# Kernel optimization log

Measured on AMD Instinct MI355X. Metric: run time of the kernel, lower is better.

Reference implementation:

```python
import jax, jax.numpy as jnp
import numpy as np

N = 100000       # nodes
E = 3200000      # edges
D_IN, D_CONV, D_LIN, D_OUT = 32, 16, 64, 4


def _uniform(k, shape, fan_in):
    s = 1.0 / np.sqrt(fan_in)
    return jax.random.uniform(k, shape, jnp.float32, -s, s)


def setup_inputs() -> dict:
    key = jax.random.key(0)
    ks = jax.random.split(key, 32)
    inp = {}
    inp["x"] = jax.random.normal(ks[0], (N, D_IN), jnp.float32)
    inp["edge_index"] = jax.random.randint(ks[1], (2, E), 0, N).astype(jnp.int64)
    conv_dims = [(D_IN, D_CONV), (D_CONV, D_CONV), (D_CONV, D_CONV)]
    j = 2
    for i, (di, do) in enumerate(conv_dims):
        inp[f"Wl{i}"] = _uniform(ks[j], (di, do), di); j += 1  # neighbor lin (lin_l)
        inp[f"Wr{i}"] = _uniform(ks[j], (di, do), di); j += 1  # root lin (lin_r, no bias)
        inp[f"bl{i}"] = _uniform(ks[j], (do,), di); j += 1
    lin_dims = [(D_CONV, D_LIN), (D_LIN, D_LIN), (D_LIN, D_LIN), (D_LIN, D_OUT)]
    for i, (di, do) in enumerate(lin_dims):
        inp[f"LW{i}"] = _uniform(ks[j], (di, do), di); j += 1
        inp[f"LB{i}"] = _uniform(ks[j], (do,), di); j += 1
    return inp


def _sage_conv(x, src, dst, Wl, Wr, b):
    # mean aggregation of source-node features at destination nodes
    msg_sum = jax.ops.segment_sum(x[src], dst, num_segments=N)          # [N, d_in]
    deg = jax.ops.segment_sum(jnp.ones((src.shape[0], 1), x.dtype), dst, num_segments=N)
    agg = msg_sum / jnp.maximum(deg, 1.0)
    return agg @ Wl + b + x @ Wr


def reference(x, edge_index,
              Wl0, Wr0, bl0, Wl1, Wr1, bl1, Wl2, Wr2, bl2,
              LW0, LB0, LW1, LB1, LW2, LB2, LW3, LB3):
    src, dst = edge_index[0], edge_index[1]
    # conv stack (dropout is identity in eval mode)
    for Wl, Wr, b in ((Wl0, Wr0, bl0), (Wl1, Wr1, bl1), (Wl2, Wr2, bl2)):
        x = jax.nn.elu(_sage_conv(x, src, dst, Wl, Wr, b))
    # hidden linear stack
    for W, b in ((LW0, LB0), (LW1, LB1), (LW2, LB2)):
        x = jax.nn.elu(x @ W + b)
    return x @ LW3 + LB3
```

## Files before the change

### kernel.cpp

```cpp
#include <hip/hip_runtime.h>
#include <hip/hip_fp16.h>
#include <math.h>

#define DCONV 16
#define BSH 8
#define GPART 512
#define GSH 9
#define MAXNB 512
#define SCAP 6912
#define FCAP 12288


__global__ void __launch_bounds__(512) k_hist(const int* __restrict__ ei, int E,
                                              int nb_buckets, int chunk,
                                              int* __restrict__ cnt) {
  __shared__ int hist[MAXNB];
  int g = blockIdx.x;
  for (int i = threadIdx.x; i < nb_buckets; i += 512) hist[i] = 0;
  __syncthreads();
  int e0 = g * chunk, e1 = min(e0 + chunk, E);
  for (int e = e0 + threadIdx.x; e < e1; e += 512)
    atomicAdd(&hist[ei[E + e] >> BSH], 1);
  __syncthreads();
  for (int i = threadIdx.x; i < nb_buckets; i += 512)
    cnt[i * GPART + g] = hist[i];
}

__global__ void k_block_sums(const int* __restrict__ in, int n, int* __restrict__ part) {
  int i = blockIdx.x * 256 + threadIdx.x;
  int v = (i < n) ? in[i] : 0;
  #pragma unroll
  for (int off = 32; off > 0; off >>= 1) v += __shfl_down(v, off, 64);
  __shared__ int ws[4];
  if ((threadIdx.x & 63) == 0) ws[threadIdx.x >> 6] = v;
  __syncthreads();
  if (threadIdx.x == 0) part[blockIdx.x] = ws[0] + ws[1] + ws[2] + ws[3];
}

__global__ void k_scan_part(int* __restrict__ part, int nb) {
  __shared__ int s[1024];
  int t = threadIdx.x;
  int v = (t < nb) ? part[t] : 0;
  s[t] = v;
  __syncthreads();
  for (int off = 1; off < 1024; off <<= 1) {
    int u = (t >= off) ? s[t - off] : 0;
    __syncthreads();
    s[t] += u;
    __syncthreads();
  }
  if (t < nb) part[t] = s[t] - v;
}

__global__ void k_excl_apply(const int* __restrict__ in, int n, const int* __restrict__ part,
                             int* __restrict__ outT, int nb_buckets) {
  __shared__ int s[256];
  int t = threadIdx.x;
  int i = blockIdx.x * 256 + t;
  int v = (i < n) ? in[i] : 0;
  s[t] = v;
  __syncthreads();
  for (int off = 1; off < 256; off <<= 1) {
    int u = (t >= off) ? s[t - off] : 0;
    __syncthreads();
    s[t] += u;
    __syncthreads();
  }
  if (i < n) {
    int excl = s[t] - v + part[blockIdx.x];
    int b = i >> GSH;
    int g = i & (GPART - 1);
    outT[g * nb_buckets + b] = excl;
  }
}

__global__ void __launch_bounds__(512) k_scatter(const int* __restrict__ ei, int E,
                                                 int nb_buckets, int chunk,
                                                 const int* __restrict__ offT,
                                                 int* __restrict__ temp) {
  __shared__ int sh[512];
  __shared__ int lofs[MAXNB];
  __shared__ int lcur[MAXNB];
  __shared__ int gbase[MAXNB];
  __shared__ int sorted[SCAP];
  __shared__ unsigned short sbkt[SCAP];
  int g = blockIdx.x, t = threadIdx.x;
  int e0 = g * chunk, e1 = min(e0 + chunk, E);
  int total = e1 - e0;

  if (total > SCAP) {
    for (int i = t; i < nb_buckets; i += 512) lcur[i] = offT[(size_t)g * nb_buckets + i];
    __syncthreads();
    for (int e = e0 + t; e < e1; e += 512) {
      int s = ei[e];
      int d = ei[E + e];
      int b = d >> BSH;
      int pos = atomicAdd(&lcur[b], 1);
      temp[pos] = (s << BSH) | (d & ((1 << BSH) - 1));
    }
    return;
  }

  lcur[t] = 0;
  __syncthreads();
  for (int e = e0 + t; e < e1; e += 512)
    atomicAdd(&lcur[ei[E + e] >> BSH], 1);
  __syncthreads();
  int v = (t < nb_buckets) ? lcur[t] : 0;
  sh[t] = v;
  __syncthreads();
  for (int off = 1; off < 512; off <<= 1) {
    int u = (t >= off) ? sh[t - off] : 0;
    __syncthreads();
    sh[t] += u;
    __syncthreads();
  }
  if (t < nb_buckets) {
    int excl = sh[t] - v;
    lofs[t] = excl;
    lcur[t] = excl;
    gbase[t] = offT[(size_t)g * nb_buckets + t];
  }
  __syncthreads();
  for (int e = e0 + t; e < e1; e += 512) {
    int s = ei[e];
    int d = ei[E + e];
    int b = d >> BSH;
    int pos = atomicAdd(&lcur[b], 1);
    sorted[pos] = (s << BSH) | (d & ((1 << BSH) - 1));
    sbkt[pos] = (unsigned short)b;
  }
  __syncthreads();
  for (int i = t; i < total; i += 512) {
    int b = sbkt[i];
    temp[gbase[b] + (i - lofs[b])] = sorted[i];
  }
}

__global__ void __launch_bounds__(512) k_fine(const int* __restrict__ temp,
                                              const int* __restrict__ offT,
                                              int nb_buckets, int E, int n,
                                              int* __restrict__ rowptr, int* __restrict__ csr) {
  __shared__ int hist[1 << BSH];
  __shared__ int cur[1 << BSH];
  __shared__ int sorted[FCAP];
  int b = blockIdx.x, t = threadIdx.x;
  int lo = offT[b];
  int hi = (b == nb_buckets - 1) ? E : offT[b + 1];
  int cntb = hi - lo;
  if (t < 256) hist[t] = 0;
  __syncthreads();
  for (int e = lo + t; e < hi; e += 512)
    atomicAdd(&hist[temp[e] & 255], 1);
  __syncthreads();
  int v = 0;
  if (t < 256) { v = hist[t]; cur[t] = v; }
  __syncthreads();
  for (int offm = 1; offm < 256; offm <<= 1) {
    int u = (t >= offm && t < 256) ? cur[t - offm] : 0;
    __syncthreads();
    if (t < 256) cur[t] += u;
    __syncthreads();
  }
  bool inlds = (cntb <= FCAP);
  if (t < 256) {
    int excl = cur[t] - v;
    int node = (b << BSH) + t;
    if (node < n) rowptr[node] = lo + excl;
    cur[t] = inlds ? excl : (lo + excl);
  }
  if (b == nb_buckets - 1 && t == 0) rowptr[n] = hi;
  __syncthreads();
  if (inlds) {
    for (int e = lo + t; e < hi; e += 512) {
      int p = temp[e];
      int pos = atomicAdd(&cur[p & 255], 1);
      sorted[pos] = p >> BSH;
    }
    __syncthreads();
    for (int i = t; i < cntb; i += 512) csr[lo + i] = sorted[i];
  } else {
    for (int e = lo + t; e < hi; e += 512) {
      int p = temp[e];
      int pos = atomicAdd(&cur[p & 255], 1);
      csr[pos] = p >> BSH;
    }
  }
}


__global__ void k_xform32h(const float* __restrict__ xin,
                           const float* __restrict__ Wl,
                           __half* __restrict__ y, int n) {
  __shared__ float sWl[32 * 16];
  int t = threadIdx.x;
  for (int i = t; i < 32 * 16; i += 256) sWl[i] = Wl[i];
  __syncthreads();
  int l = t & 15;
  int base = (t & 63) & ~15;
  int node = (blockIdx.x * 256 + t) >> 4;
  if (node >= n) return;
  float x0 = xin[node * 32 + l];
  float x1 = xin[node * 32 + 16 + l];
  float ay = 0.f;
  #pragma unroll
  for (int i = 0; i < 16; ++i) {
    float v0 = __shfl(x0, base + i, 64);
    float v1 = __shfl(x1, base + i, 64);
    ay += v0 * sWl[i * 16 + l] + v1 * sWl[(16 + i) * 16 + l];
  }
  y[node * 16 + l] = __float2half_rn(ay);
}

__global__ void k_xform16h(const float* __restrict__ hin,
                           const float* __restrict__ Wl,
                           __half* __restrict__ y, int n) {
  __shared__ float sWl[16 * 16];
  int t = threadIdx.x;
  for (int i = t; i < 16 * 16; i += 256) sWl[i] = Wl[i];
  __syncthreads();
  int l = t & 15;
  int base = (t & 63) & ~15;
  int node = (blockIdx.x * 256 + t) >> 4;
  if (node >= n) return;
  float x0 = hin[node * 16 + l];
  float ay = 0.f;
  #pragma unroll
  for (int i = 0; i < 16; ++i) {
    float v0 = __shfl(x0, base + i, 64);
    ay += v0 * sWl[i * 16 + l];
  }
  y[node * 16 + l] = __float2half_rn(ay);
}


template <int DI>
__global__ void k_agg(const __half* __restrict__ y, const float* __restrict__ hin,
                      const float* __restrict__ Wr, const float* __restrict__ bias,
                      const int* __restrict__ rowptr, const int* __restrict__ csr,
                      float* __restrict__ outp, int n) {
  __shared__ __align__(16) float sWr[DI * 16];
  __shared__ float sb[16];
  {
    int tt = threadIdx.x;
    for (int i = tt; i < DI * 16; i += 256) sWr[i] = Wr[i];
    if (tt < 16) sb[tt] = bias[tt];
  }
  __syncthreads();

  int t = blockIdx.x * 256 + threadIdx.x;
  int l = t & 3;
  int h = (t >> 2) & 1;
  int node = t >> 3;
  if (node >= n) return;
  int r0 = rowptr[node], r1 = rowptr[node + 1];
  int deg = r1 - r0;
  int halfn = (deg + 1) >> 1;
  int ks = r0 + h * halfn;
  int ke = h ? r1 : (r0 + halfn);

  const uint2* __restrict__ yv = reinterpret_cast<const uint2*>(y);

  float a0 = 0.f, a1 = 0.f, a2 = 0.f, a3 = 0.f;
  float b0 = 0.f, b1 = 0.f, b2 = 0.f, b3 = 0.f;
  float c0 = 0.f, c1 = 0.f, c2 = 0.f, c3 = 0.f;
  float d0 = 0.f, d1 = 0.f, d2 = 0.f, d3 = 0.f;
  int k = ks;
  for (; k + 3 < ke; k += 4) {
    int ia = csr[k], ib = csr[k + 1], ic = csr[k + 2], id = csr[k + 3];
    uint2 ra = yv[ia * 4 + l];
    uint2 rb = yv[ib * 4 + l];
    uint2 rc = yv[ic * 4 + l];
    uint2 rd = yv[id * 4 + l];
    float2 fa0 = __half22float2(*reinterpret_cast<const __half2*>(&ra.x));
    float2 fa1 = __half22float2(*reinterpret_cast<const __half2*>(&ra.y));
    float2 fb0 = __half22float2(*reinterpret_cast<const __half2*>(&rb.x));
    float2 fb1 = __half22float2(*reinterpret_cast<const __half2*>(&rb.y));
    float2 fc0 = __half22float2(*reinterpret_cast<const __half2*>(&rc.x));
    float2 fc1 = __half22float2(*reinterpret_cast<const __half2*>(&rc.y));
    float2 fd0 = __half22float2(*reinterpret_cast<const __half2*>(&rd.x));
    float2 fd1 = __half22float2(*reinterpret_cast<const __half2*>(&rd.y));
    a0 += fa0.x; a1 += fa0.y; a2 += fa1.x; a3 += fa1.y;
    b0 += fb0.x; b1 += fb0.y; b2 += fb1.x; b3 += fb1.y;
    c0 += fc0.x; c1 += fc0.y; c2 += fc1.x; c3 += fc1.y;
    d0 += fd0.x; d1 += fd0.y; d2 += fd1.x; d3 += fd1.y;
  }
  for (; k < ke; ++k) {
    int ia = csr[k];
    uint2 ra = yv[ia * 4 + l];
    float2 fa0 = __half22float2(*reinterpret_cast<const __half2*>(&ra.x));
    float2 fa1 = __half22float2(*reinterpret_cast<const __half2*>(&ra.y));
    a0 += fa0.x; a1 += fa0.y; a2 += fa1.x; a3 += fa1.y;
  }
  float s0 = a0 + b0 + c0 + d0;
  float s1 = a1 + b1 + c1 + d1;
  float s2 = a2 + b2 + c2 + d2;
  float s3 = a3 + b3 + c3 + d3;

  int cbase = l * 4;
  float4 rr;
  if (h == 0) rr = *reinterpret_cast<const float4*>(&sb[cbase]);
  else        rr = make_float4(0.f, 0.f, 0.f, 0.f);
  const int HD = DI / 2;
  #pragma unroll
  for (int i = 0; i < HD; ++i) {
    int ii = h * HD + i;
    float hv = hin[node * DI + ii];
    float4 w = *reinterpret_cast<const float4*>(&sWr[ii * 16 + cbase]);
    rr.x += hv * w.x; rr.y += hv * w.y; rr.z += hv * w.z; rr.w += hv * w.w;
  }

  s0 += __shfl_xor(s0, 4, 64);
  s1 += __shfl_xor(s1, 4, 64);
  s2 += __shfl_xor(s2, 4, 64);
  s3 += __shfl_xor(s3, 4, 64);
  rr.x += __shfl_xor(rr.x, 4, 64);
  rr.y += __shfl_xor(rr.y, 4, 64);
  rr.z += __shfl_xor(rr.z, 4, 64);
  rr.w += __shfl_xor(rr.w, 4, 64);

  if (h == 0) {
    float inv = 1.f / fmaxf((float)deg, 1.f);
    float ax = s0 * inv + rr.x;
    float ay = s1 * inv + rr.y;
    float az = s2 * inv + rr.z;
    float aw = s3 * inv + rr.w;
    float4 o;
    o.x = ax > 0.f ? ax : (__expf(ax) - 1.f);
    o.y = ay > 0.f ? ay : (__expf(ay) - 1.f);
    o.z = az > 0.f ? az : (__expf(az) - 1.f);
    o.w = aw > 0.f ? aw : (__expf(aw) - 1.f);
    *reinterpret_cast<float4*>(&outp[node * 16 + cbase]) = o;
  }
}


typedef _Float16 f16x4 __attribute__((ext_vector_type(4)));
typedef float f32x4 __attribute__((ext_vector_type(4)));

#define MFMA16(a, b, c) __builtin_amdgcn_mfma_f32_16x16x16f16(a, b, c, 0, 0, 0)
#define CSTRIDE 20

__global__ void __launch_bounds__(256) k_mlp(
    const float* __restrict__ xin,
    const float* __restrict__ W0, const float* __restrict__ B0,
    const float* __restrict__ W1, const float* __restrict__ B1,
    const float* __restrict__ W2, const float* __restrict__ B2,
    const float* __restrict__ W3, const float* __restrict__ B3,
    float* __restrict__ out, int n, int nchunks) {
  __shared__ __align__(16) _Float16 hbuf[4][2][64 * CSTRIDE];
  int t = threadIdx.x;
  int w = t >> 6;
  int lane = t & 63;
  int row = lane & 15;
  int kg = lane >> 4;

  f16x4 b0f[4], b1f[4][4], b2f[4][4], b3f[4];
  float bs0[4], bs1v[4], bs2v[4];
  #pragma unroll
  for (int nt = 0; nt < 4; ++nt) {
    #pragma unroll
    for (int j = 0; j < 4; ++j)
      b0f[nt][j] = (_Float16)W0[(kg * 4 + j) * 64 + nt * 16 + row];
    bs0[nt] = B0[nt * 16 + row];
    bs1v[nt] = B1[nt * 16 + row];
    bs2v[nt] = B2[nt * 16 + row];
  }
  #pragma unroll
  for (int ks = 0; ks < 4; ++ks)
    #pragma unroll
    for (int nt = 0; nt < 4; ++nt)
      #pragma unroll
      for (int j = 0; j < 4; ++j) {
        b1f[ks][nt][j] = (_Float16)W1[(ks * 16 + kg * 4 + j) * 64 + nt * 16 + row];
        b2f[ks][nt][j] = (_Float16)W2[(ks * 16 + kg * 4 + j) * 64 + nt * 16 + row];
      }
  #pragma unroll
  for (int ks = 0; ks < 4; ++ks)
    #pragma unroll
    for (int j = 0; j < 4; ++j)
      b3f[ks][j] = (row < 4) ? (_Float16)W3[(ks * 16 + kg * 4 + j) * 4 + row]
                             : (_Float16)0.f;
  float bs3 = (row < 4) ? B3[row] : 0.f;

  _Float16* hb0 = &hbuf[w][0][0];
  _Float16* hb1 = &hbuf[w][1][0];

  for (int c = blockIdx.x; c < nchunks; c += gridDim.x) {
    int nodeBase = c * 64 + w * 16;
    if (nodeBase >= n) continue;

    int nd = nodeBase + row;
    if (nd >= n) nd = n - 1;
    float4 xv = *reinterpret_cast<const float4*>(&xin[nd * 16 + kg * 4]);
    f16x4 a0;
    a0[0] = (_Float16)xv.x; a0[1] = (_Float16)xv.y;
    a0[2] = (_Float16)xv.z; a0[3] = (_Float16)xv.w;
    #pragma unroll
    for (int nt = 0; nt < 4; ++nt) {
      f32x4 acc = {bs0[nt], bs0[nt], bs0[nt], bs0[nt]};
      acc = MFMA16(a0, b0f[nt], acc);
      f16x4 hv;
      #pragma unroll
      for (int i = 0; i < 4; ++i) {
        float v = acc[i];
        v = v > 0.f ? v : (__expf(v) - 1.f);
        hv[i] = (_Float16)v;
      }
      *reinterpret_cast<f16x4*>(&hb0[(nt * 16 + row) * CSTRIDE + kg * 4]) = hv;
    }

    {
      f16x4 a[4];
      #pragma unroll
      for (int ks = 0; ks < 4; ++ks)
        #pragma unroll
        for (int j = 0; j < 4; ++j)
          a[ks][j] = hb0[(ks * 16 + kg * 4 + j) * CSTRIDE + row];
      #pragma unroll
      for (int nt = 0; nt < 4; ++nt) {
        f32x4 acc = {bs1v[nt], bs1v[nt], bs1v[nt], bs1v[nt]};
        #pragma unroll
        for (int ks = 0; ks < 4; ++ks) acc = MFMA16(a[ks], b1f[ks][nt], acc);
        f16x4 hv;
        #pragma unroll
        for (int i = 0; i < 4; ++i) {
          float v = acc[i];
          v = v > 0.f ? v : (__expf(v) - 1.f);
          hv[i] = (_Float16)v;
        }
        *reinterpret_cast<f16x4*>(&hb1[(nt * 16 + row) * CSTRIDE + kg * 4]) = hv;
      }
    }

    {
      f16x4 a[4];
      #pragma unroll
      for (int ks = 0; ks < 4; ++ks)
        #pragma unroll
        for (int j = 0; j < 4; ++j)
          a[ks][j] = hb1[(ks * 16 + kg * 4 + j) * CSTRIDE + row];
      #pragma unroll
      for (int nt = 0; nt < 4; ++nt) {
        f32x4 acc = {bs2v[nt], bs2v[nt], bs2v[nt], bs2v[nt]};
        #pragma unroll
        for (int ks = 0; ks < 4; ++ks) acc = MFMA16(a[ks], b2f[ks][nt], acc);
        f16x4 hv;
        #pragma unroll
        for (int i = 0; i < 4; ++i) {
          float v = acc[i];
          v = v > 0.f ? v : (__expf(v) - 1.f);
          hv[i] = (_Float16)v;
        }
        *reinterpret_cast<f16x4*>(&hb0[(nt * 16 + row) * CSTRIDE + kg * 4]) = hv;
      }
    }

    {
      f16x4 a[4];
      #pragma unroll
      for (int ks = 0; ks < 4; ++ks)
        #pragma unroll
        for (int j = 0; j < 4; ++j)
          a[ks][j] = hb0[(ks * 16 + kg * 4 + j) * CSTRIDE + row];
      f32x4 acc = {bs3, bs3, bs3, bs3};
      #pragma unroll
      for (int ks = 0; ks < 4; ++ks) acc = MFMA16(a[ks], b3f[ks], acc);
      if (row < 4) {
        #pragma unroll
        for (int i = 0; i < 4; ++i) {
          int nd2 = nodeBase + kg * 4 + i;
          if (nd2 < n) out[nd2 * 4 + row] = acc[i];
        }
      }
    }
  }
}


extern "C" void kernel_launch(void* const* d_in, const int* in_sizes, int n_in,
                              void* d_out, int out_size, void* d_ws, size_t ws_size,
                              hipStream_t stream) {
  const float* x   = (const float*)d_in[0];
  const int*   ei  = (const int*)d_in[1];
  const float* Wl0 = (const float*)d_in[2];
  const float* Wr0 = (const float*)d_in[3];
  const float* bl0 = (const float*)d_in[4];
  const float* Wl1 = (const float*)d_in[5];
  const float* Wr1 = (const float*)d_in[6];
  const float* bl1 = (const float*)d_in[7];
  const float* Wl2 = (const float*)d_in[8];
  const float* Wr2 = (const float*)d_in[9];
  const float* bl2 = (const float*)d_in[10];
  const float* LW0 = (const float*)d_in[11];
  const float* LB0 = (const float*)d_in[12];
  const float* LW1 = (const float*)d_in[13];
  const float* LB1 = (const float*)d_in[14];
  const float* LW2 = (const float*)d_in[15];
  const float* LB2 = (const float*)d_in[16];
  const float* LW3 = (const float*)d_in[17];
  const float* LB3 = (const float*)d_in[18];
  float* out = (float*)d_out;

  const int N_ = in_sizes[0] / 32;
  const int E_ = in_sizes[1] / 2;

  const int NB = (N_ + (1 << BSH) - 1) >> BSH;
  const int chunk = (E_ + GPART - 1) / GPART;
  const int n2 = NB * GPART;
  const int nb2 = (n2 + 255) / 256;

  char* wsp = (char*)d_ws;
  int* cnt    = (int*)wsp;  wsp += sizeof(int) * (size_t)n2;
  int* offT   = (int*)wsp;  wsp += sizeof(int) * (size_t)n2;
  int* part   = (int*)wsp;  wsp += sizeof(int) * 1024;
  int* temp   = (int*)wsp;  wsp += sizeof(int) * (size_t)E_;
  int* csr    = (int*)wsp;  wsp += sizeof(int) * (size_t)E_;
  size_t hBytes = sizeof(float) * (size_t)N_ * DCONV;
  float* Ha   = (float*)wsp; wsp += hBytes;
  int* rowptr = (int*)wsp;  wsp += sizeof(int) * (size_t)(N_ + 1);
  __half* y16 = (__half*)temp;
  float*  Hb  = (float*)((char*)temp + sizeof(__half) * (size_t)N_ * DCONV);

  k_hist<<<GPART, 512, 0, stream>>>(ei, E_, NB, chunk, cnt);
  k_block_sums<<<nb2, 256, 0, stream>>>(cnt, n2, part);
  k_scan_part<<<1, 1024, 0, stream>>>(part, nb2);
  k_excl_apply<<<nb2, 256, 0, stream>>>(cnt, n2, part, offT, NB);
  k_scatter<<<GPART, 512, 0, stream>>>(ei, E_, NB, chunk, offT, temp);
  k_fine<<<NB, 512, 0, stream>>>(temp, offT, NB, E_, N_, rowptr, csr);

  int nbX = (N_ * 16 + 255) / 256;
  int nbA = (N_ * 8 + 255) / 256;

  k_xform32h<<<nbX, 256, 0, stream>>>(x, Wl0, y16, N_);
  k_agg<32><<<nbA, 256, 0, stream>>>(y16, x, Wr0, bl0, rowptr, csr, Ha, N_);
  k_xform16h<<<nbX, 256, 0, stream>>>(Ha, Wl1, y16, N_);
  k_agg<16><<<nbA, 256, 0, stream>>>(y16, Ha, Wr1, bl1, rowptr, csr, Hb, N_);
  k_xform16h<<<nbX, 256, 0, stream>>>(Hb, Wl2, y16, N_);
  k_agg<16><<<nbA, 256, 0, stream>>>(y16, Hb, Wr2, bl2, rowptr, csr, Ha, N_);

  int nchunks = (N_ + 63) / 64;
  int nbM = 512;
  if (nbM > nchunks) nbM = nchunks;
  k_mlp<<<nbM, 256, 0, stream>>>(Ha, LW0, LB0, LW1, LB1, LW2, LB2, LW3, LB3, out, N_, nchunks);
}
```

Measured before the change: 177.3 us.

## Fuse next-layer neighbor transform into aggregation and split edges four ways per node

The separate 16x16 transform kernels are removed. Each aggregation kernel now also computes the next layer's fp16 neighbor projection from its ELU output, using wave shuffles. The aggregation also assigns 16 threads per node instead of 8, so each node's edge list is split into quarters for more parallelism on the gather. This saves two kernel launches and a read/write pass over the hidden features. In exchange it adds shuffle work, puts the next layer's y in a separate ping-pong buffer, and lowers per-thread edge work on low-degree nodes.

After: 171.7 us. -3.2%, faster.

```diff
diff --git a/kernel.cpp b/kernel.cpp
--- a/kernel.cpp
+++ b/kernel.cpp
@@ -212,52 +212,34 @@
   y[node * 16 + l] = __float2half_rn(ay);
 }
 
-__global__ void k_xform16h(const float* __restrict__ hin,
-                           const float* __restrict__ Wl,
-                           __half* __restrict__ y, int n) {
-  __shared__ float sWl[16 * 16];
-  int t = threadIdx.x;
-  for (int i = t; i < 16 * 16; i += 256) sWl[i] = Wl[i];
-  __syncthreads();
-  int l = t & 15;
-  int base = (t & 63) & ~15;
-  int node = (blockIdx.x * 256 + t) >> 4;
-  if (node >= n) return;
-  float x0 = hin[node * 16 + l];
-  float ay = 0.f;
-  #pragma unroll
-  for (int i = 0; i < 16; ++i) {
-    float v0 = __shfl(x0, base + i, 64);
-    ay += v0 * sWl[i * 16 + l];
-  }
-  y[node * 16 + l] = __float2half_rn(ay);
-}
-
-
-template <int DI>
+
+template <int DI, bool FUSE>
 __global__ void k_agg(const __half* __restrict__ y, const float* __restrict__ hin,
                       const float* __restrict__ Wr, const float* __restrict__ bias,
+                      const float* __restrict__ Wlnext,
                       const int* __restrict__ rowptr, const int* __restrict__ csr,
-                      float* __restrict__ outp, int n) {
+                      float* __restrict__ outp, __half* __restrict__ ynext, int n) {
   __shared__ __align__(16) float sWr[DI * 16];
   __shared__ float sb[16];
+  __shared__ float sWl[16 * 16];
   {
     int tt = threadIdx.x;
     for (int i = tt; i < DI * 16; i += 256) sWr[i] = Wr[i];
     if (tt < 16) sb[tt] = bias[tt];
+    if (FUSE) sWl[tt] = Wlnext[tt];
   }
   __syncthreads();
 
   int t = blockIdx.x * 256 + threadIdx.x;
   int l = t & 3;
-  int h = (t >> 2) & 1;
-  int node = t >> 3;
+  int q = (t >> 2) & 3;
+  int node = t >> 4;
   if (node >= n) return;
   int r0 = rowptr[node], r1 = rowptr[node + 1];
   int deg = r1 - r0;
-  int halfn = (deg + 1) >> 1;
-  int ks = r0 + h * halfn;
-  int ke = h ? r1 : (r0 + halfn);
+  int quarter = (deg + 3) >> 2;
+  int ks = r0 + q * quarter;
+  int ke = min(ks + quarter, r1);
 
   const uint2* __restrict__ yv = reinterpret_cast<const uint2*>(y);
 
@@ -292,45 +274,67 @@
     float2 fa1 = __half22float2(*reinterpret_cast<const __half2*>(&ra.y));
     a0 += fa0.x; a1 += fa0.y; a2 += fa1.x; a3 += fa1.y;
   }
-  float s0 = a0 + b0 + c0 + d0;
-  float s1 = a1 + b1 + c1 + d1;
-  float s2 = a2 + b2 + c2 + d2;
-  float s3 = a3 + b3 + c3 + d3;
+  float s0 = (a0 + b0) + (c0 + d0);
+  float s1 = (a1 + b1) + (c1 + d1);
+  float s2 = (a2 + b2) + (c2 + d2);
+  float s3 = (a3 + b3) + (c3 + d3);
 
   int cbase = l * 4;
   float4 rr;
-  if (h == 0) rr = *reinterpret_cast<const float4*>(&sb[cbase]);
+  if (q == 0) rr = *reinterpret_cast<const float4*>(&sb[cbase]);
   else        rr = make_float4(0.f, 0.f, 0.f, 0.f);
-  const int HD = DI / 2;
-  #pragma unroll
-  for (int i = 0; i < HD; ++i) {
-    int ii = h * HD + i;
+  const int QD = DI / 4;
+  #pragma unroll
+  for (int i = 0; i < QD; ++i) {
+    int ii = q * QD + i;
     float hv = hin[node * DI + ii];
     float4 w = *reinterpret_cast<const float4*>(&sWr[ii * 16 + cbase]);
     rr.x += hv * w.x; rr.y += hv * w.y; rr.z += hv * w.z; rr.w += hv * w.w;
   }
 
-  s0 += __shfl_xor(s0, 4, 64);
-  s1 += __shfl_xor(s1, 4, 64);
-  s2 += __shfl_xor(s2, 4, 64);
-  s3 += __shfl_xor(s3, 4, 64);
-  rr.x += __shfl_xor(rr.x, 4, 64);
-  rr.y += __shfl_xor(rr.y, 4, 64);
-  rr.z += __shfl_xor(rr.z, 4, 64);
-  rr.w += __shfl_xor(rr.w, 4, 64);
-
-  if (h == 0) {
-    float inv = 1.f / fmaxf((float)deg, 1.f);
-    float ax = s0 * inv + rr.x;
-    float ay = s1 * inv + rr.y;
-    float az = s2 * inv + rr.z;
-    float aw = s3 * inv + rr.w;
-    float4 o;
-    o.x = ax > 0.f ? ax : (__expf(ax) - 1.f);
-    o.y = ay > 0.f ? ay : (__expf(ay) - 1.f);
-    o.z = az > 0.f ? az : (__expf(az) - 1.f);
-    o.w = aw > 0.f ? aw : (__expf(aw) - 1.f);
+  #pragma unroll
+  for (int m = 4; m <= 8; m <<= 1) {
+    s0 += __shfl_xor(s0, m, 64);
+    s1 += __shfl_xor(s1, m, 64);
+    s2 += __shfl_xor(s2, m, 64);
+    s3 += __shfl_xor(s3, m, 64);
+    rr.x += __shfl_xor(rr.x, m, 64);
+    rr.y += __shfl_xor(rr.y, m, 64);
+    rr.z += __shfl_xor(rr.z, m, 64);
+    rr.w += __shfl_xor(rr.w, m, 64);
+  }
+
+  float inv = 1.f / fmaxf((float)deg, 1.f);
+  float ax = s0 * inv + rr.x;
+  float ay = s1 * inv + rr.y;
+  float az = s2 * inv + rr.z;
+  float aw = s3 * inv + rr.w;
+  float4 o;
+  o.x = ax > 0.f ? ax : (__expf(ax) - 1.f);
+  o.y = ay > 0.f ? ay : (__expf(ay) - 1.f);
+  o.z = az > 0.f ? az : (__expf(az) - 1.f);
+  o.w = aw > 0.f ? aw : (__expf(aw) - 1.f);
+  if (q == 0) {
     *reinterpret_cast<float4*>(&outp[node * 16 + cbase]) = o;
+  }
+
+  if (FUSE) {
+    int c = t & 15;
+    int grpbase = (threadIdx.x & 63) & ~15;
+    float acc = 0.f;
+    #pragma unroll
+    for (int i = 0; i < 16; ++i) {
+      int src = grpbase + (i >> 2);
+      float hv;
+      switch (i & 3) {
+        case 0: hv = __shfl(o.x, src, 64); break;
+        case 1: hv = __shfl(o.y, src, 64); break;
+        case 2: hv = __shfl(o.z, src, 64); break;
+        default: hv = __shfl(o.w, src, 64); break;
+      }
+      acc += hv * sWl[i * 16 + c];
+    }
+    ynext[node * 16 + c] = __float2half_rn(acc);
   }
 }
 
@@ -519,8 +523,10 @@
   size_t hBytes = sizeof(float) * (size_t)N_ * DCONV;
   float* Ha   = (float*)wsp; wsp += hBytes;
   int* rowptr = (int*)wsp;  wsp += sizeof(int) * (size_t)(N_ + 1);
-  __half* y16 = (__half*)temp;
-  float*  Hb  = (float*)((char*)temp + sizeof(__half) * (size_t)N_ * DCONV);
+  size_t yBytes = sizeof(__half) * (size_t)N_ * DCONV;
+  __half* y16a = (__half*)temp;
+  __half* y16b = (__half*)((char*)temp + yBytes);
+  float*  Hb   = (float*)((char*)temp + 2 * yBytes);
 
   k_hist<<<GPART, 512, 0, stream>>>(ei, E_, NB, chunk, cnt);
   k_block_sums<<<nb2, 256, 0, stream>>>(cnt, n2, part);
@@ -530,14 +536,12 @@
   k_fine<<<NB, 512, 0, stream>>>(temp, offT, NB, E_, N_, rowptr, csr);
 
   int nbX = (N_ * 16 + 255) / 256;
-  int nbA = (N_ * 8 + 255) / 256;
-
-  k_xform32h<<<nbX, 256, 0, stream>>>(x, Wl0, y16, N_);
-  k_agg<32><<<nbA, 256, 0, stream>>>(y16, x, Wr0, bl0, rowptr, csr, Ha, N_);
-  k_xform16h<<<nbX, 256, 0, stream>>>(Ha, Wl1, y16, N_);
-  k_agg<16><<<nbA, 256, 0, stream>>>(y16, Ha, Wr1, bl1, rowptr, csr, Hb, N_);
-  k_xform16h<<<nbX, 256, 0, stream>>>(Hb, Wl2, y16, N_);
-  k_agg<16><<<nbA, 256, 0, stream>>>(y16, Hb, Wr2, bl2, rowptr, csr, Ha, N_);
+  int nbA = (N_ * 16 + 255) / 256;
+
+  k_xform32h<<<nbX, 256, 0, stream>>>(x, Wl0, y16a, N_);
+  k_agg<32, true><<<nbA, 256, 0, stream>>>(y16a, x, Wr0, bl0, Wl1, rowptr, csr, Ha, y16b, N_);
+  k_agg<16, true><<<nbA, 256, 0, stream>>>(y16b, Ha, Wr1, bl1, Wl2, rowptr, csr, Hb, y16a, N_);
+  k_agg<16, false><<<nbA, 256, 0, stream>>>(y16a, Hb, Wr2, bl2, nullptr, rowptr, csr, Ha, nullptr, N_);
 
   int nchunks = (N_ + 63) / 64;
   int nbM = 512;
```
